# Kernel tuning notes

Hardware: AMD Instinct MI355X
Metric: run time of the kernel (lower is better)

## Reference

```python
import jax, jax.numpy as jnp
import numpy as np

LAYERS = [3, 1024, 512, 256, 128, 1]
WIDTHS = [3, 1024, 1024, 1024, 1024, 1]  # width per BsPINN: 2^(i-1)*Layers[i]
N = 131072


def _mask(num_blocks, bs1, bs2):
    # block-diagonal mask of ones, built statically (constant under jit)
    return jnp.asarray(np.kron(np.eye(num_blocks, dtype=np.float32),
                               np.ones((bs1, bs2), dtype=np.float32)))


def _xavier(key, shape, fan_in, fan_out):
    lim = np.sqrt(6.0 / (fan_in + fan_out)).astype(np.float32)
    return jax.random.uniform(key, shape, jnp.float32, -lim, lim)


def setup_inputs() -> dict:
    key = jax.random.key(0)
    ks = jax.random.split(key, 6)
    inp = {
        "X": jax.random.uniform(ks[0], (N, 3), dtype=jnp.float32),
        "lb_X": jnp.zeros((3,), jnp.float32),
        "ub_X": jnp.ones((3,), jnp.float32),
    }
    for i in range(5):
        # xavier scale per sub-block Layers[i] x Layers[i+1], as in the torch init
        inp[f"W{i}"] = _xavier(ks[i + 1], (WIDTHS[i], WIDTHS[i + 1]),
                               LAYERS[i], LAYERS[i + 1])
        inp[f"b{i}"] = jnp.zeros((1, WIDTHS[i + 1]), jnp.float32)
    return inp


def reference(X, lb_X, ub_X, W0, b0, W1, b1, W2, b2, W3, b3, W4, b4):
    # masks for hidden layers l=2,3: 2 blocks of 512x512, 4 blocks of 256x256
    m2 = _mask(2, LAYERS[2], 2 * LAYERS[3])   # [1024,1024]
    m3 = _mask(4, LAYERS[3], 2 * LAYERS[4])   # [1024,1024]
    h = 2.0 * (X - lb_X) / (ub_X - lb_X) - 1.0  # [N,3]
    h = jnp.sin(h @ W0 + b0)            # [N,1024] dense
    h = jnp.sin(h @ W1 + b1)            # [N,1024] dense
    h = jnp.sin(h @ (W2 * m2) + b2)     # [N,1024] block-diag (2 blocks)
    h = jnp.sin(h @ (W3 * m3) + b3)     # [N,1024] block-diag (4 blocks)
    return h @ W4 + b4                  # [N,1]
```

## Files before the change

### kernel.cpp

```cpp
#include <hip/hip_runtime.h>

typedef _Float16 f16x8 __attribute__((ext_vector_type(8)));
typedef _Float16 f16x4 __attribute__((ext_vector_type(4)));
typedef __fp16  fp16x2 __attribute__((ext_vector_type(2)));
typedef float f32x4 __attribute__((ext_vector_type(4)));
typedef unsigned int u32;

#define ROWS 64
#define THREADS 512

__global__ __launch_bounds__(512) void pack_weights(
    const float* __restrict__ W1, const float* __restrict__ W2,
    const float* __restrict__ W3, _Float16* __restrict__ WF1,
    _Float16* __restrict__ WF2, _Float16* __restrict__ WF3) {
  int t = blockIdx.x * 512 + threadIdx.x;
  const float* src; _Float16* dst; int idx, ct, kt, lane, kbase;
  if (t < 131072) {
    idx = t; src = W1; dst = WF1;
    ct = idx >> 11; kt = (idx >> 6) & 31; lane = idx & 63; kbase = 0;
  } else if (t < 196608) {
    idx = t - 131072; src = W2; dst = WF2;
    ct = idx >> 10; kt = (idx >> 6) & 15; lane = idx & 63;
    kbase = (ct >= 32) ? 512 : 0;
  } else {
    idx = t - 196608; src = W3; dst = WF3;
    ct = idx >> 9; kt = (idx >> 6) & 7; lane = idx & 63;
    kbase = (ct >> 4) << 8;
  }
  int c  = ct * 16 + (lane & 15);
  int k0 = kbase + kt * 32 + ((lane >> 4) << 3);
  f16x8 v;
#pragma unroll
  for (int j = 0; j < 8; ++j) v[j] = (_Float16)src[(size_t)(k0 + j) * 1024 + c];
  *reinterpret_cast<f16x8*>(dst + (size_t)idx * 8) = v;
}

template <int KTFULL>
__device__ __forceinline__ void kloop(const _Float16* __restrict__ WF, char* hb,
                                      f32x4 (&acc)[4][4], int ct0, int lane,
                                      int nkt, u32 ldsk0) {
  const f16x8* wf = reinterpret_cast<const f16x8*>(WF) +
                    (u32)(ct0 * KTFULL * 64 + lane);
  const int arow = lane & 15;
  const int koff = (lane >> 4) << 3;
  const u32 abase = (u32)(arow * 2048);
  const u32 axor  = (u32)(arow << 4);

  f16x8 wA[4], wB[4], hA[4], hB[4];
#define LOADW(buf, ktv)                                                        \
  { u32 _kt = (u32)(ktv);                                                      \
    _Pragma("unroll") for (int cf = 0; cf < 4; ++cf)                           \
      buf[cf] = wf[(u32)(cf * KTFULL) * 64u + _kt * 64u]; }
#define LDH(buf, ktv)                                                          \
  { u32 kb = ldsk0 + (u32)((ktv) * 64) + (u32)(koff * 2);                      \
    _Pragma("unroll") for (int rf = 0; rf < 4; ++rf) {                         \
      u32 addr = ((u32)(rf * 32768) + abase + kb) ^ axor;                      \
      buf[rf] = *reinterpret_cast<const f16x8*>(hb + addr);                    \
    } }
#define DOMFMA(w, h)                                                           \
  { _Pragma("unroll") for (int cf = 0; cf < 4; ++cf)                           \
      _Pragma("unroll") for (int rf = 0; rf < 4; ++rf)                         \
        acc[cf][rf] = __builtin_amdgcn_mfma_f32_16x16x32_f16(w[cf], h[rf],     \
                                                             acc[cf][rf], 0, 0, 0); }

  LOADW(wA, 0);
  LDH(hA, 0);
#pragma unroll 1
  for (int kt = 0; kt < nkt; kt += 2) {
    int ktn = (kt + 2 < nkt) ? (kt + 2) : 0;
    LOADW(wB, kt + 1);
    LDH(hB, kt + 1);
    DOMFMA(wA, hA);
    LOADW(wA, ktn);
    LDH(hA, ktn);
    DOMFMA(wB, hB);
  }
#undef LOADW
#undef LDH
#undef DOMFMA
}

__global__
__attribute__((amdgpu_flat_work_group_size(512, 512), amdgpu_waves_per_eu(2, 2)))
void bspinn_fused(
    const float* __restrict__ X, const float* __restrict__ lb,
    const float* __restrict__ ub,
    const float* __restrict__ W0, const float* __restrict__ b0,
    const _Float16* __restrict__ WF1, const float* __restrict__ b1,
    const _Float16* __restrict__ WF2, const float* __restrict__ b2,
    const _Float16* __restrict__ WF3, const float* __restrict__ b3,
    const float* __restrict__ W4, const float* __restrict__ b4,
    float* __restrict__ out) {
  __shared__ alignas(16) char hb[ROWS * 2048];
  __shared__ float xs[ROWS * 4];
  __shared__ float partials[8 * ROWS];

  const int tid  = threadIdx.x;
  const int lane = tid & 63;
  const int wid  = tid >> 6;
  const int r0   = blockIdx.x * ROWS;

  if (tid < ROWS * 3) {
    int r = tid / 3, j = tid - r * 3;
    float x = X[(size_t)r0 * 3 + tid];
    xs[r * 4 + j] = 2.0f * (x - lb[j]) / (ub[j] - lb[j]) - 1.0f;
  }
  __syncthreads();

  {
    int c0 = tid * 2;
    float wa0 = W0[c0],        wb0 = W0[c0 + 1];
    float wa1 = W0[1024 + c0], wb1 = W0[1025 + c0];
    float wa2 = W0[2048 + c0], wb2 = W0[2049 + c0];
    float ba = b0[c0], bbv = b0[c0 + 1];
#pragma unroll 4
    for (int r = 0; r < ROWS; ++r) {
      float x0 = xs[r * 4], x1 = xs[r * 4 + 1], x2 = xs[r * 4 + 2];
      float va = __sinf(fmaf(x2, wa2, fmaf(x1, wa1, fmaf(x0, wa0, ba))));
      float vb = __sinf(fmaf(x2, wb2, fmaf(x1, wb1, fmaf(x0, wb0, bbv))));
      union { fp16x2 h2; u32 u; } pk;
      pk.h2 = __builtin_amdgcn_cvt_pkrtz(va, vb);
      u32 addr = ((u32)(r * 2048 + c0 * 2)) ^ ((u32)((r & 15) << 4));
      *reinterpret_cast<u32*>(hb + addr) = pk.u;
    }
  }
  __syncthreads();

  const int csub = (lane >> 4) << 2;
  const int rr   = lane & 15;
  f32x4 acc[4][4];
  f16x4 p1[4][4], p2[4][4];

  auto zacc = [&]() {
#pragma unroll
    for (int cf = 0; cf < 4; ++cf)
#pragma unroll
      for (int rf = 0; rf < 4; ++rf) acc[cf][rf] = f32x4{0.f, 0.f, 0.f, 0.f};
  };
  auto epi_regs = [&](f16x4 (&p)[4][4], const float* bias, int c0w) {
#pragma unroll
    for (int cf = 0; cf < 4; ++cf) {
      int c0 = c0w + cf * 16 + csub;
      f32x4 bb = *reinterpret_cast<const f32x4*>(bias + c0);
#pragma unroll
      for (int rf = 0; rf < 4; ++rf) {
        float s0 = __sinf(acc[cf][rf][0] + bb[0]);
        float s1 = __sinf(acc[cf][rf][1] + bb[1]);
        float s2 = __sinf(acc[cf][rf][2] + bb[2]);
        float s3 = __sinf(acc[cf][rf][3] + bb[3]);
        union { fp16x2 h2[2]; f16x4 v; } pk;
        pk.h2[0] = __builtin_amdgcn_cvt_pkrtz(s0, s1);
        pk.h2[1] = __builtin_amdgcn_cvt_pkrtz(s2, s3);
        p[cf][rf] = pk.v;
      }
    }
  };
  auto store_regs = [&](f16x4 (&p)[4][4], int c0w) {
#pragma unroll
    for (int cf = 0; cf < 4; ++cf) {
      int c0 = c0w + cf * 16 + csub;
#pragma unroll
      for (int rf = 0; rf < 4; ++rf) {
        int r = rf * 16 + rr;
        u32 addr = ((u32)(r * 2048 + c0 * 2)) ^ ((u32)(rr << 4));
        *reinterpret_cast<f16x4*>(hb + addr) = p[cf][rf];
      }
    }
  };

  const int cw0 = wid * 64;
  const int cw1 = 512 + wid * 64;
  const int ct00 = wid * 4, ct01 = 32 + wid * 4;

  zacc(); kloop<32>(WF1, hb, acc, ct00, lane, 32, 0);
  epi_regs(p1, b1, cw0);
  zacc(); kloop<32>(WF1, hb, acc, ct01, lane, 32, 0);
  epi_regs(p2, b1, cw1);
  __syncthreads();
  store_regs(p1, cw0); store_regs(p2, cw1);
  __syncthreads();

  zacc(); kloop<16>(WF2, hb, acc, ct00, lane, 16, 0);
  epi_regs(p1, b2, cw0);
  zacc(); kloop<16>(WF2, hb, acc, ct01, lane, 16, 1024);
  epi_regs(p2, b2, cw1);
  __syncthreads();
  store_regs(p1, cw0); store_regs(p2, cw1);
  __syncthreads();

  {
    u32 k0a = (u32)(((wid >> 2)) * 512);
    u32 k0b = (u32)((2 + (wid >> 2)) * 512);
    zacc(); kloop<8>(WF3, hb, acc, ct00, lane, 8, k0a);
    epi_regs(p1, b3, cw0);
    zacc(); kloop<8>(WF3, hb, acc, ct01, lane, 8, k0b);
    epi_regs(p2, b3, cw1);
    __syncthreads();
    store_regs(p1, cw0); store_regs(p2, cw1);
    __syncthreads();
  }

  {
    int r = lane, seg = wid;
    u32 rb = (u32)(r * 2048);
    u32 xr = (u32)((r & 15) << 4);
    float s = 0.f;
#pragma unroll
    for (int kk = 0; kk < 128; kk += 8) {
      int k = seg * 128 + kk;
      f16x8 v = *reinterpret_cast<const f16x8*>(hb + ((rb + (u32)(k * 2)) ^ xr));
#pragma unroll
      for (int j = 0; j < 8; ++j) s = fmaf((float)v[j], W4[k + j], s);
    }
    partials[seg * 64 + r] = s;
  }
  __syncthreads();
  if (tid < ROWS) {
    float s = b4[0];
#pragma unroll
    for (int g = 0; g < 8; ++g) s += partials[g * 64 + tid];
    out[r0 + tid] = s;
  }
}

extern "C" void kernel_launch(void* const* d_in, const int* in_sizes, int n_in,
                              void* d_out, int out_size, void* d_ws, size_t ws_size,
                              hipStream_t stream) {
  const float* X  = (const float*)d_in[0];
  const float* lb = (const float*)d_in[1];
  const float* ub = (const float*)d_in[2];
  const float* W0 = (const float*)d_in[3];
  const float* b0 = (const float*)d_in[4];
  const float* W1 = (const float*)d_in[5];
  const float* b1 = (const float*)d_in[6];
  const float* W2 = (const float*)d_in[7];
  const float* b2 = (const float*)d_in[8];
  const float* W3 = (const float*)d_in[9];
  const float* b3 = (const float*)d_in[10];
  const float* W4 = (const float*)d_in[11];
  const float* b4 = (const float*)d_in[12];
  float* out = (float*)d_out;

  _Float16* WF1 = (_Float16*)d_ws;
  _Float16* WF2 = (_Float16*)((char*)d_ws + 2097152);
  _Float16* WF3 = (_Float16*)((char*)d_ws + 3145728);

  hipLaunchKernelGGL(pack_weights, dim3(448), dim3(512), 0, stream,
                     W1, W2, W3, WF1, WF2, WF3);
  hipLaunchKernelGGL(bspinn_fused, dim3(131072 / ROWS), dim3(THREADS), 0, stream,
                     X, lb, ub, W0, b0, WF1, b1, WF2, b2, WF3, b3, W4, b4, out);
}
```

Before: 504.1 us.

## Interleave first-half sine epilogue into second-half MFMA k-loop with setprio

Each layer's second column-half GEMM now runs in a fused k-loop that computes slices of the first half's sine/pack epilogue between MFMA groups. The aim is to overlap transcendental VALU work with matrix-core work instead of running them back to back. MFMA groups are also wrapped in s_setprio to favour matrix issue. In exchange, two accumulator sets stay live, raising register pressure at 2 waves/EU, and the new fused loop drops the double-buffered prefetch used by the plain loop.

Measured after the change: 539.7 us. 7.1% more time.

```diff
diff --git a/kernel.cpp b/kernel.cpp
--- a/kernel.cpp
+++ b/kernel.cpp
@@ -36,9 +36,10 @@
 }
 
 template <int KTFULL>
-__device__ __forceinline__ void kloop(const _Float16* __restrict__ WF, char* hb,
-                                      f32x4 (&acc)[4][4], int ct0, int lane,
-                                      int nkt, u32 ldsk0) {
+__device__ __forceinline__ void kloop_plain(const _Float16* __restrict__ WF,
+                                            char* hb, f32x4 (&acc)[4][4],
+                                            int ct0, int lane, int nkt,
+                                            u32 ldsk0) {
   const f16x8* wf = reinterpret_cast<const f16x8*>(WF) +
                     (u32)(ct0 * KTFULL * 64 + lane);
   const int arow = lane & 15;
@@ -58,10 +59,12 @@
       buf[rf] = *reinterpret_cast<const f16x8*>(hb + addr);                    \
     } }
 #define DOMFMA(w, h)                                                           \
-  { _Pragma("unroll") for (int cf = 0; cf < 4; ++cf)                           \
+  { __builtin_amdgcn_s_setprio(1);                                             \
+    _Pragma("unroll") for (int cf = 0; cf < 4; ++cf)                           \
       _Pragma("unroll") for (int rf = 0; rf < 4; ++rf)                         \
         acc[cf][rf] = __builtin_amdgcn_mfma_f32_16x16x32_f16(w[cf], h[rf],     \
-                                                             acc[cf][rf], 0, 0, 0); }
+                                                             acc[cf][rf], 0, 0, 0); \
+    __builtin_amdgcn_s_setprio(0); }
 
   LOADW(wA, 0);
   LDH(hA, 0);
@@ -78,6 +81,74 @@
 #undef LOADW
 #undef LDH
 #undef DOMFMA
+}
+
+template <int KTFULL, int NKT>
+__device__ __forceinline__ void kloop_fused(const _Float16* __restrict__ WF,
+                                            char* hb, f32x4 (&acc)[4][4],
+                                            int ct0, int lane, u32 ldsk0,
+                                            f32x4 (&accP)[4][4],
+                                            f16x4 (&park)[4][4],
+                                            const f32x4 (&bb)[4]) {
+  const f16x8* wf = reinterpret_cast<const f16x8*>(WF) +
+                    (u32)(ct0 * KTFULL * 64 + lane);
+  const int arow = lane & 15;
+  const int koff = (lane >> 4) << 3;
+  const u32 abase = (u32)(arow * 2048);
+  const u32 axor  = (u32)(arow << 4);
+
+#define SL(S) { const int cfS = (S) >> 2, rfS = (S) & 3;                       \
+    float s0 = __sinf(accP[cfS][rfS][0] + bb[cfS][0]);                         \
+    float s1 = __sinf(accP[cfS][rfS][1] + bb[cfS][1]);                         \
+    float s2 = __sinf(accP[cfS][rfS][2] + bb[cfS][2]);                         \
+    float s3 = __sinf(accP[cfS][rfS][3] + bb[cfS][3]);                         \
+    union { fp16x2 h2[2]; f16x4 v; } pk;                                       \
+    pk.h2[0] = __builtin_amdgcn_cvt_pkrtz(s0, s1);                             \
+    pk.h2[1] = __builtin_amdgcn_cvt_pkrtz(s2, s3);                             \
+    park[cfS][rfS] = pk.v; }
+
+  auto slice = [&](int s) {
+    switch (s) {
+      case 0:  SL(0)  break; case 1:  SL(1)  break; case 2:  SL(2)  break;
+      case 3:  SL(3)  break; case 4:  SL(4)  break; case 5:  SL(5)  break;
+      case 6:  SL(6)  break; case 7:  SL(7)  break; case 8:  SL(8)  break;
+      case 9:  SL(9)  break; case 10: SL(10) break; case 11: SL(11) break;
+      case 12: SL(12) break; case 13: SL(13) break; case 14: SL(14) break;
+      default: SL(15) break;
+    }
+  };
+
+#pragma unroll 1
+  for (int kt = 0; kt < NKT; ++kt) {
+    f16x8 w[4];
+#pragma unroll
+    for (int cf = 0; cf < 4; ++cf)
+      w[cf] = wf[(u32)(cf * KTFULL) * 64u + (u32)kt * 64u];
+    u32 kb = ldsk0 + (u32)(kt * 64) + (u32)(koff * 2);
+    f16x8 h[4];
+#pragma unroll
+    for (int rf = 0; rf < 4; ++rf) {
+      u32 addr = ((u32)(rf * 32768) + abase + kb) ^ axor;
+      h[rf] = *reinterpret_cast<const f16x8*>(hb + addr);
+    }
+    __builtin_amdgcn_s_setprio(1);
+#pragma unroll
+    for (int cf = 0; cf < 4; ++cf)
+#pragma unroll
+      for (int rf = 0; rf < 4; ++rf)
+        acc[cf][rf] = __builtin_amdgcn_mfma_f32_16x16x32_f16(w[cf], h[rf],
+                                                             acc[cf][rf], 0, 0, 0);
+    __builtin_amdgcn_s_setprio(0);
+    if constexpr (NKT == 32) {
+      if ((kt & 1) == 0) slice(kt >> 1);
+    } else if constexpr (NKT == 16) {
+      slice(kt);
+    } else {
+      slice(kt * 2);
+      slice(kt * 2 + 1);
+    }
+  }
+#undef SL
 }
 
 __global__
@@ -128,26 +199,32 @@
 
   const int csub = (lane >> 4) << 2;
   const int rr   = lane & 15;
-  f32x4 acc[4][4];
+  f32x4 acc1[4][4], acc2[4][4];
   f16x4 p1[4][4], p2[4][4];
-
-  auto zacc = [&]() {
+  f32x4 bb[4];
+
+  auto zacc = [&](f32x4 (&a)[4][4]) {
 #pragma unroll
     for (int cf = 0; cf < 4; ++cf)
 #pragma unroll
-      for (int rf = 0; rf < 4; ++rf) acc[cf][rf] = f32x4{0.f, 0.f, 0.f, 0.f};
-  };
-  auto epi_regs = [&](f16x4 (&p)[4][4], const float* bias, int c0w) {
+      for (int rf = 0; rf < 4; ++rf) a[cf][rf] = f32x4{0.f, 0.f, 0.f, 0.f};
+  };
+  auto loadbias = [&](const float* bias, int c0w) {
+#pragma unroll
+    for (int cf = 0; cf < 4; ++cf)
+      bb[cf] = *reinterpret_cast<const f32x4*>(bias + c0w + cf * 16 + csub);
+  };
+  auto epi_regs = [&](f32x4 (&a)[4][4], f16x4 (&p)[4][4], const float* bias,
+                      int c0w) {
 #pragma unroll
     for (int cf = 0; cf < 4; ++cf) {
-      int c0 = c0w + cf * 16 + csub;
-      f32x4 bb = *reinterpret_cast<const f32x4*>(bias + c0);
+      f32x4 bv = *reinterpret_cast<const f32x4*>(bias + c0w + cf * 16 + csub);
 #pragma unroll
       for (int rf = 0; rf < 4; ++rf) {
-        float s0 = __sinf(acc[cf][rf][0] + bb[0]);
-        float s1 = __sinf(acc[cf][rf][1] + bb[1]);
-        float s2 = __sinf(acc[cf][rf][2] + bb[2]);
-        float s3 = __sinf(acc[cf][rf][3] + bb[3]);
+        float s0 = __sinf(a[cf][rf][0] + bv[0]);
+        float s1 = __sinf(a[cf][rf][1] + bv[1]);
+        float s2 = __sinf(a[cf][rf][2] + bv[2]);
+        float s3 = __sinf(a[cf][rf][3] + bv[3]);
         union { fp16x2 h2[2]; f16x4 v; } pk;
         pk.h2[0] = __builtin_amdgcn_cvt_pkrtz(s0, s1);
         pk.h2[1] = __builtin_amdgcn_cvt_pkrtz(s2, s3);
@@ -172,18 +249,22 @@
   const int cw1 = 512 + wid * 64;
   const int ct00 = wid * 4, ct01 = 32 + wid * 4;
 
-  zacc(); kloop<32>(WF1, hb, acc, ct00, lane, 32, 0);
-  epi_regs(p1, b1, cw0);
-  zacc(); kloop<32>(WF1, hb, acc, ct01, lane, 32, 0);
-  epi_regs(p2, b1, cw1);
+  zacc(acc1);
+  kloop_plain<32>(WF1, hb, acc1, ct00, lane, 32, 0);
+  loadbias(b1, cw0);
+  zacc(acc2);
+  kloop_fused<32, 32>(WF1, hb, acc2, ct01, lane, 0, acc1, p1, bb);
+  epi_regs(acc2, p2, b1, cw1);
   __syncthreads();
   store_regs(p1, cw0); store_regs(p2, cw1);
   __syncthreads();
 
-  zacc(); kloop<16>(WF2, hb, acc, ct00, lane, 16, 0);
-  epi_regs(p1, b2, cw0);
-  zacc(); kloop<16>(WF2, hb, acc, ct01, lane, 16, 1024);
-  epi_regs(p2, b2, cw1);
+  zacc(acc1);
+  kloop_plain<16>(WF2, hb, acc1, ct00, lane, 16, 0);
+  loadbias(b2, cw0);
+  zacc(acc2);
+  kloop_fused<16, 16>(WF2, hb, acc2, ct01, lane, 1024, acc1, p1, bb);
+  epi_regs(acc2, p2, b2, cw1);
   __syncthreads();
   store_regs(p1, cw0); store_regs(p2, cw1);
   __syncthreads();
@@ -191,10 +272,12 @@
   {
     u32 k0a = (u32)(((wid >> 2)) * 512);
     u32 k0b = (u32)((2 + (wid >> 2)) * 512);
-    zacc(); kloop<8>(WF3, hb, acc, ct00, lane, 8, k0a);
-    epi_regs(p1, b3, cw0);
-    zacc(); kloop<8>(WF3, hb, acc, ct01, lane, 8, k0b);
-    epi_regs(p2, b3, cw1);
+    zacc(acc1);
+    kloop_plain<8>(WF3, hb, acc1, ct00, lane, 8, k0a);
+    loadbias(b3, cw0);
+    zacc(acc2);
+    kloop_fused<8, 8>(WF3, hb, acc2, ct01, lane, k0b, acc1, p1, bb);
+    epi_regs(acc2, p2, b3, cw1);
     __syncthreads();
     store_regs(p1, cw0); store_regs(p2, cw1);
     __syncthreads();
```
